# Kernel tuning notes

Hardware: AMD Instinct MI355X
Metric: run time of the kernel (lower is better)

The kernel has to match this reference:

```python
import jax, jax.numpy as jnp
import numpy as np

N_NODES = 100000
N_EDGES = 3200000
N_IN = 512
N_H = 256

def setup_inputs() -> dict:
    key = jax.random.key(0)
    ks = jax.random.split(key, 8)
    features = jax.random.normal(ks[0], (N_NODES, N_IN), dtype=jnp.float32)
    src = jax.random.randint(ks[1], (N_EDGES,), 0, N_NODES, dtype=jnp.int32)
    dst = jax.random.randint(ks[2], (N_EDGES,), 0, N_NODES, dtype=jnp.int32)
    W1 = jax.random.normal(ks[3], (N_IN, N_H), dtype=jnp.float32) / np.sqrt(N_IN)
    b1 = jnp.zeros((N_H,), dtype=jnp.float32)
    a1 = jnp.full((N_H,), 0.25, dtype=jnp.float32)  # PReLU init
    W2 = jax.random.normal(ks[4], (N_H, N_H), dtype=jnp.float32) / np.sqrt(N_H)
    b2 = jnp.zeros((N_H,), dtype=jnp.float32)
    a2 = jnp.full((N_H,), 0.25, dtype=jnp.float32)
    return {"features": features, "src": src, "dst": dst,
            "W1": W1, "b1": b1, "a1": a1, "W2": W2, "b2": b2, "a2": a2}

def _degree_norms(src, dst, n_nodes):
    ones = jnp.ones(src.shape[0], dtype=jnp.float32)
    out_deg = jax.ops.segment_sum(ones, src, num_segments=n_nodes)
    in_deg = jax.ops.segment_sum(ones, dst, num_segments=n_nodes)
    # DGL clamps degree to min 1 for norm='both'
    norm_src = jax.lax.rsqrt(jnp.maximum(out_deg, 1.0))  # [N]
    norm_dst = jax.lax.rsqrt(jnp.maximum(in_deg, 1.0))   # [N]
    return norm_src, norm_dst

def _graph_conv(x, src, dst, norm_src, norm_dst, W, b, a):
    # DGL GraphConv norm='both': h = Dd^-1/2 * A^T (Ds^-1/2 * x W) + b, then PReLU
    h = (x * norm_src[:, None]) @ W                     # [N, out]
    agg = jax.ops.segment_sum(h[src], dst, num_segments=x.shape[0])  # SpMM gather/scatter
    h = agg * norm_dst[:, None] + b
    return jnp.maximum(h, 0.0) + a * jnp.minimum(h, 0.0)  # PReLU per-channel

def reference(features, src, dst, W1, b1, a1, W2, b2, a2):
    norm_src, norm_dst = _degree_norms(src, dst, features.shape[0])
    h = _graph_conv(features, src, dst, norm_src, norm_dst, W1, b1, a1)
    h = _graph_conv(h, src, dst, norm_src, norm_dst, W2, b2, a2)
    return h
```

## Files before the change

kernel.cpp:

```cpp
#include <hip/hip_runtime.h>
#include <hip/hip_bf16.h>

typedef unsigned short u16;
typedef short s16x8 __attribute__((ext_vector_type(8)));
typedef u16 u16x4 __attribute__((ext_vector_type(4)));
typedef u16 u16x8 __attribute__((ext_vector_type(8)));
typedef float f32x4 __attribute__((ext_vector_type(4)));

#define BSHIFT 10

__device__ __forceinline__ u16 f2bf(float f) {
    __hip_bfloat16 b = __float2bfloat16(f);
    return __builtin_bit_cast(u16, b);
}
__device__ __forceinline__ float bf2f(u16 u) {
    unsigned int x = ((unsigned int)u) << 16;
    return __builtin_bit_cast(float, x);
}


__global__ __launch_bounds__(256) void bhist_k(const int* __restrict__ src,
                                               const int* __restrict__ dst,
                                               int* __restrict__ bcntA,
                                               int* __restrict__ bcntB,
                                               int E, int chunk) {
    __shared__ int hA[128], hB[128];
    const int base = blockIdx.x * chunk;
    const int end = (base + chunk) < E ? (base + chunk) : E;
    if (threadIdx.x < 128) { hA[threadIdx.x] = 0; hB[threadIdx.x] = 0; }
    __syncthreads();
    for (int i = base + threadIdx.x; i < end; i += 256) {
        atomicAdd(&hA[dst[i] >> BSHIFT], 1);
        atomicAdd(&hB[src[i] >> BSHIFT], 1);
    }
    __syncthreads();
    if (threadIdx.x < 128) {
        if (hA[threadIdx.x]) atomicAdd(&bcntA[threadIdx.x], hA[threadIdx.x]);
        if (hB[threadIdx.x]) atomicAdd(&bcntB[threadIdx.x], hB[threadIdx.x]);
    }
}

__global__ void bscan_k(const int* __restrict__ bcntA, const int* __restrict__ bcntB,
                        int* __restrict__ bbaseA, int* __restrict__ bbaseB,
                        int* __restrict__ bcurA, int* __restrict__ bcurB,
                        int* __restrict__ row_ptr, int NB, int N, int E) {
    __shared__ int tA[128], tB[128];
    const int t = threadIdx.x;
    int vA = (t < NB) ? bcntA[t] : 0;
    int vB = (t < NB) ? bcntB[t] : 0;
    tA[t] = vA; tB[t] = vB;
    __syncthreads();
    for (int d = 1; d < 128; d <<= 1) {
        int aA = (t >= d) ? tA[t - d] : 0;
        int aB = (t >= d) ? tB[t - d] : 0;
        __syncthreads();
        tA[t] += aA; tB[t] += aB;
        __syncthreads();
    }
    if (t < NB) {
        int eA = tA[t] - vA, eB = tB[t] - vB;
        bbaseA[t] = eA; bcurA[t] = eA;
        bbaseB[t] = eB; bcurB[t] = eB;
    } else if (t == NB) {
        bbaseA[NB] = E; bbaseB[NB] = E;
    }
    if (t == 0) row_ptr[N] = E;
}

__global__ __launch_bounds__(256) void part_k(const int* __restrict__ src,
                                              const int* __restrict__ dst,
                                              int* __restrict__ bcurA,
                                              int* __restrict__ bcurB,
                                              int2* __restrict__ pairs,
                                              int* __restrict__ sb,
                                              int E, int chunk) {
    __shared__ int hA[128], hB[128];
    const int base = blockIdx.x * chunk;
    const int end = (base + chunk) < E ? (base + chunk) : E;
    if (threadIdx.x < 128) { hA[threadIdx.x] = 0; hB[threadIdx.x] = 0; }
    __syncthreads();
    for (int i = base + threadIdx.x; i < end; i += 256) {
        atomicAdd(&hA[dst[i] >> BSHIFT], 1);
        atomicAdd(&hB[src[i] >> BSHIFT], 1);
    }
    __syncthreads();
    if (threadIdx.x < 128) {
        int c = hA[threadIdx.x];
        hA[threadIdx.x] = c ? atomicAdd(&bcurA[threadIdx.x], c) : 0;
        c = hB[threadIdx.x];
        hB[threadIdx.x] = c ? atomicAdd(&bcurB[threadIdx.x], c) : 0;
    }
    __syncthreads();
    for (int i = base + threadIdx.x; i < end; i += 256) {
        int d = dst[i], s = src[i];
        int posA = atomicAdd(&hA[d >> BSHIFT], 1);
        int2 pr; pr.x = s; pr.y = d;
        pairs[posA] = pr;
        int posB = atomicAdd(&hB[s >> BSHIFT], 1);
        sb[posB] = s;
    }
}

__global__ __launch_bounds__(256) void bcsr_k(const int2* __restrict__ pairs,
                                              const int* __restrict__ bbase,
                                              int* __restrict__ row_ptr,
                                              int* __restrict__ din,
                                              int* __restrict__ col, int N) {
    __shared__ int hist[1024];
    __shared__ int cur[1024];
    __shared__ int psum[256];
    const int b = blockIdx.x;
    const int beg = bbase[b], end = bbase[b + 1];
    const int nbase = b << BSHIFT;
    const int nlen = (N - nbase) < 1024 ? (N - nbase) : 1024;
    const int t = threadIdx.x;
#pragma unroll
    for (int j = 0; j < 4; j++) hist[t * 4 + j] = 0;
    __syncthreads();
    for (int i = beg + t; i < end; i += 256)
        atomicAdd(&hist[pairs[i].y - nbase], 1);
    __syncthreads();
    int h0 = hist[4 * t], h1 = hist[4 * t + 1], h2 = hist[4 * t + 2], h3 = hist[4 * t + 3];
    int s = h0 + h1 + h2 + h3;
    psum[t] = s;
    __syncthreads();
    for (int d = 1; d < 256; d <<= 1) {
        int add = (t >= d) ? psum[t - d] : 0;
        __syncthreads();
        psum[t] += add;
        __syncthreads();
    }
    int e0 = psum[t] - s;
    int e1 = e0 + h0, e2 = e1 + h1, e3 = e2 + h2;
    cur[4 * t] = beg + e0; cur[4 * t + 1] = beg + e1;
    cur[4 * t + 2] = beg + e2; cur[4 * t + 3] = beg + e3;
    if (4 * t + 0 < nlen) { row_ptr[nbase + 4 * t + 0] = beg + e0; din[nbase + 4 * t + 0] = h0; }
    if (4 * t + 1 < nlen) { row_ptr[nbase + 4 * t + 1] = beg + e1; din[nbase + 4 * t + 1] = h1; }
    if (4 * t + 2 < nlen) { row_ptr[nbase + 4 * t + 2] = beg + e2; din[nbase + 4 * t + 2] = h2; }
    if (4 * t + 3 < nlen) { row_ptr[nbase + 4 * t + 3] = beg + e3; din[nbase + 4 * t + 3] = h3; }
    __syncthreads();
    for (int i = beg + t; i < end; i += 256) {
        int2 p = pairs[i];
        int pos = atomicAdd(&cur[p.y - nbase], 1);
        col[pos] = p.x;
    }
}

__global__ __launch_bounds__(256) void bdeg_k(const int* __restrict__ sb,
                                              const int* __restrict__ bbase,
                                              int* __restrict__ dout, int N) {
    __shared__ int hist[1024];
    const int b = blockIdx.x;
    const int beg = bbase[b], end = bbase[b + 1];
    const int nbase = b << BSHIFT;
    const int nlen = (N - nbase) < 1024 ? (N - nbase) : 1024;
    for (int i = threadIdx.x; i < 1024; i += 256) hist[i] = 0;
    __syncthreads();
    for (int i = beg + threadIdx.x; i < end; i += 256)
        atomicAdd(&hist[sb[i] - nbase], 1);
    __syncthreads();
    for (int i = threadIdx.x; i < nlen; i += 256) dout[nbase + i] = hist[i];
}

__global__ void norms_k(const int* __restrict__ dout, const int* __restrict__ din,
                        float* __restrict__ ns, float* __restrict__ nd, int n) {
    int i = blockIdx.x * blockDim.x + threadIdx.x;
    if (i < n) {
        ns[i] = 1.0f / sqrtf(fmaxf((float)dout[i], 1.0f));
        nd[i] = 1.0f / sqrtf(fmaxf((float)din[i], 1.0f));
    }
}

__global__ void convt_k(const float* __restrict__ W, u16* __restrict__ Wt, int K, int Nn) {
    int i = blockIdx.x * blockDim.x + threadIdx.x;
    if (i < K * Nn) {
        int n = i / K, k = i - n * K;
        Wt[i] = f2bf(W[(size_t)k * Nn + n]);
    }
}


template <int K, bool AF32>
__global__ __launch_bounds__(256) void gemm_k(const void* __restrict__ Ap,
                                              const float* __restrict__ nsrc,
                                              const u16* __restrict__ Bt,
                                              u16* __restrict__ C, int M) {
    constexpr int BMt = 128, BKt = 64;
    __shared__ u16 Al[BMt * BKt];
    __shared__ u16 Bl[128 * BKt];
    const int tid = threadIdx.x, lane = tid & 63, wid = tid >> 6;
    const int wr = wid >> 1, wc = wid & 1;
    const int l15 = lane & 15, lhi = lane >> 4;
    const int bm = blockIdx.x * BMt, bn = blockIdx.y * 128;
    f32x4 acc[4][4] = {};

    for (int k0 = 0; k0 < K; k0 += BKt) {
#pragma unroll
        for (int i = 0; i < 4; i++) {
            int G = i * 256 + tid, row = G >> 3, gk = G & 7;
            int grow = bm + row;
            grow = grow < M ? grow : M - 1;
            u16x8 w;
            if constexpr (AF32) {
                const float* A = (const float*)Ap;
                const f32x4 v0 = *(const f32x4*)(A + (size_t)grow * K + k0 + gk * 8);
                const f32x4 v1 = *(const f32x4*)(A + (size_t)grow * K + k0 + gk * 8 + 4);
                const float ns = nsrc[grow];
                w[0] = f2bf(v0[0] * ns); w[1] = f2bf(v0[1] * ns);
                w[2] = f2bf(v0[2] * ns); w[3] = f2bf(v0[3] * ns);
                w[4] = f2bf(v1[0] * ns); w[5] = f2bf(v1[1] * ns);
                w[6] = f2bf(v1[2] * ns); w[7] = f2bf(v1[3] * ns);
            } else {
                const u16* A = (const u16*)Ap;
                w = *(const u16x8*)(A + (size_t)grow * K + k0 + gk * 8);
            }
            int idx = (row * BKt + gk * 8) ^ ((row & 7) << 3);
            *(u16x8*)(Al + idx) = w;
            u16x8 wb = *(const u16x8*)(Bt + (size_t)(bn + row) * K + k0 + gk * 8);
            *(u16x8*)(Bl + idx) = wb;
        }
        __syncthreads();

        s16x8 af[2][4], bfr[2][4];
#pragma unroll
        for (int kk = 0; kk < 2; kk++) {
#pragma unroll
            for (int mi = 0; mi < 4; mi++) {
                int row = wr * 64 + mi * 16 + l15;
                int idx = (row * BKt + kk * 32 + lhi * 8) ^ ((row & 7) << 3);
                af[kk][mi] = *(const s16x8*)(Al + idx);
            }
#pragma unroll
            for (int ni = 0; ni < 4; ni++) {
                int n = wc * 64 + ni * 16 + l15;
                int idx = (n * BKt + kk * 32 + lhi * 8) ^ ((n & 7) << 3);
                bfr[kk][ni] = *(const s16x8*)(Bl + idx);
            }
        }
#pragma unroll
        for (int kk = 0; kk < 2; kk++)
#pragma unroll
            for (int mi = 0; mi < 4; mi++)
#pragma unroll
                for (int ni = 0; ni < 4; ni++)
                    acc[mi][ni] = __builtin_amdgcn_mfma_f32_16x16x32_bf16(
                        af[kk][mi], bfr[kk][ni], acc[mi][ni], 0, 0, 0);
        __syncthreads();
    }

#pragma unroll
    for (int mi = 0; mi < 4; mi++) {
#pragma unroll
        for (int r = 0; r < 4; r++) {
            int grow = bm + wr * 64 + mi * 16 + lhi * 4 + r;
            if (grow < M) {
#pragma unroll
                for (int ni = 0; ni < 4; ni++) {
                    int gcol = bn + wc * 64 + ni * 16 + l15;
                    C[(size_t)grow * 256 + gcol] = f2bf(acc[mi][ni][r]);
                }
            }
        }
    }
}


__global__ __launch_bounds__(256) void agg_k(const u16* __restrict__ h,
                                             const int* __restrict__ rp,
                                             const int* __restrict__ col,
                                             const float* __restrict__ nd,
                                             const float* __restrict__ bias,
                                             const float* __restrict__ alpha,
                                             const float* __restrict__ ns,
                                             u16* __restrict__ obf, float* __restrict__ of,
                                             int n) {
    int w = (blockIdx.x * blockDim.x + threadIdx.x) >> 6;
    if (w >= n) return;
    const int lane = threadIdx.x & 63;
    const int half = lane >> 5, c0 = (lane & 31) * 8;
    const int beg = rp[w], end = rp[w + 1];

    float a0[8] = {}, a1[8] = {}, a2[8] = {}, a3[8] = {};

    int p = beg + half;
    for (; p + 6 < end; p += 8) {
        int s0 = col[p], s1 = col[p + 2], s2 = col[p + 4], s3 = col[p + 6];
        u16x8 v0 = *(const u16x8*)(h + (size_t)s0 * 256 + c0);
        u16x8 v1 = *(const u16x8*)(h + (size_t)s1 * 256 + c0);
        u16x8 v2 = *(const u16x8*)(h + (size_t)s2 * 256 + c0);
        u16x8 v3 = *(const u16x8*)(h + (size_t)s3 * 256 + c0);
#pragma unroll
        for (int j = 0; j < 8; j++) {
            a0[j] += bf2f(v0[j]);
            a1[j] += bf2f(v1[j]);
            a2[j] += bf2f(v2[j]);
            a3[j] += bf2f(v3[j]);
        }
    }
    for (; p < end; p += 2) {
        int s = col[p];
        u16x8 v = *(const u16x8*)(h + (size_t)s * 256 + c0);
#pragma unroll
        for (int j = 0; j < 8; j++) a0[j] += bf2f(v[j]);
    }
#pragma unroll
    for (int j = 0; j < 8; j++) a0[j] += (a1[j] + a2[j]) + a3[j];
#pragma unroll
    for (int j = 0; j < 8; j++) a0[j] += __shfl_xor(a0[j], 32);

    const float ndv = nd[w];
    const f32x4 bv0 = *(const f32x4*)(bias + c0);
    const f32x4 bv1 = *(const f32x4*)(bias + c0 + 4);
    const f32x4 al0 = *(const f32x4*)(alpha + c0);
    const f32x4 al1 = *(const f32x4*)(alpha + c0 + 4);
    float bb[8] = {bv0[0], bv0[1], bv0[2], bv0[3], bv1[0], bv1[1], bv1[2], bv1[3]};
    float aa[8] = {al0[0], al0[1], al0[2], al0[3], al1[0], al1[1], al1[2], al1[3]};
#pragma unroll
    for (int j = 0; j < 8; j++) {
        float s = a0[j] * ndv + bb[j];
        a0[j] = s > 0.f ? s : aa[j] * s;
    }

    if (half == 0) {
        if (obf) {
            const float nsv = ns[w];
            u16x8 o;
#pragma unroll
            for (int j = 0; j < 8; j++) o[j] = f2bf(a0[j] * nsv);
            *(u16x8*)(obf + (size_t)w * 256 + c0) = o;
        } else {
            f32x4 o0, o1;
            o0[0] = a0[0]; o0[1] = a0[1]; o0[2] = a0[2]; o0[3] = a0[3];
            o1[0] = a0[4]; o1[1] = a0[5]; o1[2] = a0[6]; o1[3] = a0[7];
            *(f32x4*)(of + (size_t)w * 256 + c0) = o0;
            *(f32x4*)(of + (size_t)w * 256 + c0 + 4) = o1;
        }
    }
}


extern "C" void kernel_launch(void* const* d_in, const int* in_sizes, int n_in,
                              void* d_out, int out_size, void* d_ws, size_t ws_size,
                              hipStream_t stream) {
    const float* feat = (const float*)d_in[0];
    const int* src = (const int*)d_in[1];
    const int* dst = (const int*)d_in[2];
    const float* W1 = (const float*)d_in[3];
    const float* b1 = (const float*)d_in[4];
    const float* a1 = (const float*)d_in[5];
    const float* W2 = (const float*)d_in[6];
    const float* b2 = (const float*)d_in[7];
    const float* a2 = (const float*)d_in[8];
    float* out = (float*)d_out;

    const int N = in_sizes[0] / 512;
    const int E = in_sizes[1];
    const int NB = (N + (1 << BSHIFT) - 1) >> BSHIFT;

    char* ws = (char*)d_ws;
    size_t off = 0;
    auto take = [&](size_t bytes) {
        size_t o = off;
        off += (bytes + 255) & ~(size_t)255;
        return o;
    };
    int* deg_out = (int*)(ws + take((size_t)N * 4));
    int* deg_in = (int*)(ws + take((size_t)N * 4));
    float* nsrc = (float*)(ws + take((size_t)N * 4));
    float* ndst = (float*)(ws + take((size_t)N * 4));
    int* row_ptr = (int*)(ws + take((size_t)(N + 1) * 4));
    int* bcnt = (int*)(ws + take(1024));
    int* bcntA = bcnt, * bcntB = bcnt + 128;
    int* bbaseA = (int*)(ws + take(512));
    int* bbaseB = (int*)(ws + take(512));
    int* bcurA = (int*)(ws + take(512));
    int* bcurB = (int*)(ws + take(512));
    int* col = (int*)(ws + take((size_t)E * 4));
    u16* W1t = (u16*)(ws + take((size_t)512 * 256 * 2));
    u16* W2t = (u16*)(ws + take((size_t)256 * 256 * 2));
    u16* h = (u16*)(ws + take((size_t)N * 256 * 2));
    u16* x2 = (u16*)(ws + take((size_t)N * 256 * 2));
    int2* pairs = (int2*)h;
    int* sb = (int*)x2;

    hipMemsetAsync(bcnt, 0, 1024, stream);

    const int chunk = 4096;
    bhist_k<<<(E + chunk - 1) / chunk, 256, 0, stream>>>(src, dst, bcntA, bcntB, E, chunk);
    bscan_k<<<1, 128, 0, stream>>>(bcntA, bcntB, bbaseA, bbaseB, bcurA, bcurB, row_ptr, NB, N, E);
    part_k<<<(E + chunk - 1) / chunk, 256, 0, stream>>>(src, dst, bcurA, bcurB, pairs, sb, E, chunk);
    bcsr_k<<<NB, 256, 0, stream>>>(pairs, bbaseA, row_ptr, deg_in, col, N);
    bdeg_k<<<NB, 256, 0, stream>>>(sb, bbaseB, deg_out, N);
    norms_k<<<(N + 255) / 256, 256, 0, stream>>>(deg_out, deg_in, nsrc, ndst, N);

    convt_k<<<(512 * 256 + 255) / 256, 256, 0, stream>>>(W1, W1t, 512, 256);
    convt_k<<<(256 * 256 + 255) / 256, 256, 0, stream>>>(W2, W2t, 256, 256);

    dim3 gg((N + 127) / 128, 2);
    int aggBlocks = (N * 64 + 255) / 256;

    gemm_k<512, true><<<gg, 256, 0, stream>>>(feat, nsrc, W1t, h, N);
    agg_k<<<aggBlocks, 256, 0, stream>>>(h, row_ptr, col, ndst, b1, a1, nsrc, x2, nullptr, N);
    gemm_k<256, false><<<gg, 256, 0, stream>>>(x2, nullptr, W2t, h, N);
    agg_k<<<aggBlocks, 256, 0, stream>>>(h, row_ptr, col, ndst, b2, a2, nullptr, nullptr, out, N);
}
```

Measured before the change: 759.3 us.

## Widen GEMM tile to full N and use half-wave per node in aggregation

```diff
diff --git a/kernel.cpp b/kernel.cpp
--- a/kernel.cpp
+++ b/kernel.cpp
@@ -181,23 +181,23 @@
 
 
 template <int K, bool AF32>
-__global__ __launch_bounds__(256) void gemm_k(const void* __restrict__ Ap,
+__global__ __launch_bounds__(512) void gemm_k(const void* __restrict__ Ap,
                                               const float* __restrict__ nsrc,
                                               const u16* __restrict__ Bt,
                                               u16* __restrict__ C, int M) {
-    constexpr int BMt = 128, BKt = 64;
-    __shared__ u16 Al[BMt * BKt];
-    __shared__ u16 Bl[128 * BKt];
+    constexpr int BKt = 64;
+    __shared__ u16 Al[128 * BKt];
+    __shared__ u16 Bl[256 * BKt];
     const int tid = threadIdx.x, lane = tid & 63, wid = tid >> 6;
-    const int wr = wid >> 1, wc = wid & 1;
+    const int wr = wid >> 2, wc = wid & 3;
     const int l15 = lane & 15, lhi = lane >> 4;
-    const int bm = blockIdx.x * BMt, bn = blockIdx.y * 128;
+    const int bm = blockIdx.x * 128;
     f32x4 acc[4][4] = {};
 
     for (int k0 = 0; k0 < K; k0 += BKt) {
 #pragma unroll
-        for (int i = 0; i < 4; i++) {
-            int G = i * 256 + tid, row = G >> 3, gk = G & 7;
+        for (int i = 0; i < 2; i++) {
+            int G = i * 512 + tid, row = G >> 3, gk = G & 7;
             int grow = bm + row;
             grow = grow < M ? grow : M - 1;
             u16x8 w;
@@ -216,7 +216,12 @@
             }
             int idx = (row * BKt + gk * 8) ^ ((row & 7) << 3);
             *(u16x8*)(Al + idx) = w;
-            u16x8 wb = *(const u16x8*)(Bt + (size_t)(bn + row) * K + k0 + gk * 8);
+        }
+#pragma unroll
+        for (int i = 0; i < 4; i++) {
+            int G = i * 512 + tid, row = G >> 3, gk = G & 7;
+            u16x8 wb = *(const u16x8*)(Bt + (size_t)row * K + k0 + gk * 8);
+            int idx = (row * BKt + gk * 8) ^ ((row & 7) << 3);
             *(u16x8*)(Bl + idx) = wb;
         }
         __syncthreads();
@@ -256,7 +261,7 @@
             if (grow < M) {
 #pragma unroll
                 for (int ni = 0; ni < 4; ni++) {
-                    int gcol = bn + wc * 64 + ni * 16 + l15;
+                    int gcol = wc * 64 + ni * 16 + l15;
                     C[(size_t)grow * 256 + gcol] = f2bf(acc[mi][ni][r]);
                 }
             }
@@ -274,21 +279,25 @@
                                              const float* __restrict__ ns,
                                              u16* __restrict__ obf, float* __restrict__ of,
                                              int n) {
-    int w = (blockIdx.x * blockDim.x + threadIdx.x) >> 6;
+    int w = (blockIdx.x * blockDim.x + threadIdx.x) >> 5;
     if (w >= n) return;
-    const int lane = threadIdx.x & 63;
-    const int half = lane >> 5, c0 = (lane & 31) * 8;
+    const int c0 = (threadIdx.x & 31) * 8;
     const int beg = rp[w], end = rp[w + 1];
 
     float a0[8] = {}, a1[8] = {}, a2[8] = {}, a3[8] = {};
 
-    int p = beg + half;
-    for (; p + 6 < end; p += 8) {
-        int s0 = col[p], s1 = col[p + 2], s2 = col[p + 4], s3 = col[p + 6];
+    int p = beg;
+    for (; p + 7 < end; p += 8) {
+        int s0 = col[p], s1 = col[p + 1], s2 = col[p + 2], s3 = col[p + 3];
+        int s4 = col[p + 4], s5 = col[p + 5], s6 = col[p + 6], s7 = col[p + 7];
         u16x8 v0 = *(const u16x8*)(h + (size_t)s0 * 256 + c0);
         u16x8 v1 = *(const u16x8*)(h + (size_t)s1 * 256 + c0);
         u16x8 v2 = *(const u16x8*)(h + (size_t)s2 * 256 + c0);
         u16x8 v3 = *(const u16x8*)(h + (size_t)s3 * 256 + c0);
+        u16x8 v4 = *(const u16x8*)(h + (size_t)s4 * 256 + c0);
+        u16x8 v5 = *(const u16x8*)(h + (size_t)s5 * 256 + c0);
+        u16x8 v6 = *(const u16x8*)(h + (size_t)s6 * 256 + c0);
+        u16x8 v7 = *(const u16x8*)(h + (size_t)s7 * 256 + c0);
 #pragma unroll
         for (int j = 0; j < 8; j++) {
             a0[j] += bf2f(v0[j]);
@@ -296,17 +305,36 @@
             a2[j] += bf2f(v2[j]);
             a3[j] += bf2f(v3[j]);
         }
-    }
-    for (; p < end; p += 2) {
+#pragma unroll
+        for (int j = 0; j < 8; j++) {
+            a0[j] += bf2f(v4[j]);
+            a1[j] += bf2f(v5[j]);
+            a2[j] += bf2f(v6[j]);
+            a3[j] += bf2f(v7[j]);
+        }
+    }
+    for (; p + 3 < end; p += 4) {
+        int s0 = col[p], s1 = col[p + 1], s2 = col[p + 2], s3 = col[p + 3];
+        u16x8 v0 = *(const u16x8*)(h + (size_t)s0 * 256 + c0);
+        u16x8 v1 = *(const u16x8*)(h + (size_t)s1 * 256 + c0);
+        u16x8 v2 = *(const u16x8*)(h + (size_t)s2 * 256 + c0);
+        u16x8 v3 = *(const u16x8*)(h + (size_t)s3 * 256 + c0);
+#pragma unroll
+        for (int j = 0; j < 8; j++) {
+            a0[j] += bf2f(v0[j]);
+            a1[j] += bf2f(v1[j]);
+            a2[j] += bf2f(v2[j]);
+            a3[j] += bf2f(v3[j]);
+        }
+    }
+    for (; p < end; p++) {
         int s = col[p];
         u16x8 v = *(const u16x8*)(h + (size_t)s * 256 + c0);
 #pragma unroll
         for (int j = 0; j < 8; j++) a0[j] += bf2f(v[j]);
     }
 #pragma unroll
-    for (int j = 0; j < 8; j++) a0[j] += (a1[j] + a2[j]) + a3[j];
-#pragma unroll
-    for (int j = 0; j < 8; j++) a0[j] += __shfl_xor(a0[j], 32);
+    for (int j = 0; j < 8; j++) a0[j] = (a0[j] + a1[j]) + (a2[j] + a3[j]);
 
     const float ndv = nd[w];
     const f32x4 bv0 = *(const f32x4*)(bias + c0);
@@ -321,20 +349,18 @@
         a0[j] = s > 0.f ? s : aa[j] * s;
     }
 
-    if (half == 0) {
-        if (obf) {
-            const float nsv = ns[w];
-            u16x8 o;
-#pragma unroll
-            for (int j = 0; j < 8; j++) o[j] = f2bf(a0[j] * nsv);
-            *(u16x8*)(obf + (size_t)w * 256 + c0) = o;
-        } else {
-            f32x4 o0, o1;
-            o0[0] = a0[0]; o0[1] = a0[1]; o0[2] = a0[2]; o0[3] = a0[3];
-            o1[0] = a0[4]; o1[1] = a0[5]; o1[2] = a0[6]; o1[3] = a0[7];
-            *(f32x4*)(of + (size_t)w * 256 + c0) = o0;
-            *(f32x4*)(of + (size_t)w * 256 + c0 + 4) = o1;
-        }
+    if (obf) {
+        const float nsv = ns[w];
+        u16x8 o;
+#pragma unroll
+        for (int j = 0; j < 8; j++) o[j] = f2bf(a0[j] * nsv);
+        *(u16x8*)(obf + (size_t)w * 256 + c0) = o;
+    } else {
+        f32x4 o0, o1;
+        o0[0] = a0[0]; o0[1] = a0[1]; o0[2] = a0[2]; o0[3] = a0[3];
+        o1[0] = a0[4]; o1[1] = a0[5]; o1[2] = a0[6]; o1[3] = a0[7];
+        *(f32x4*)(of + (size_t)w * 256 + c0) = o0;
+        *(f32x4*)(of + (size_t)w * 256 + c0 + 4) = o1;
     }
 }
 
@@ -396,11 +422,11 @@
     convt_k<<<(512 * 256 + 255) / 256, 256, 0, stream>>>(W1, W1t, 512, 256);
     convt_k<<<(256 * 256 + 255) / 256, 256, 0, stream>>>(W2, W2t, 256, 256);
 
-    dim3 gg((N + 127) / 128, 2);
-    int aggBlocks = (N * 64 + 255) / 256;
-
-    gemm_k<512, true><<<gg, 256, 0, stream>>>(feat, nsrc, W1t, h, N);
+    dim3 gg((N + 127) / 128);
+    int aggBlocks = (N * 32 + 255) / 256;
+
+    gemm_k<512, true><<<gg, 512, 0, stream>>>(feat, nsrc, W1t, h, N);
     agg_k<<<aggBlocks, 256, 0, stream>>>(h, row_ptr, col, ndst, b1, a1, nsrc, x2, nullptr, N);
-    gemm_k<256, false><<<gg, 256, 0, stream>>>(x2, nullptr, W2t, h, N);
+    gemm_k<256, false><<<gg, 512, 0, stream>>>(x2, nullptr, W2t, h, N);
     agg_k<<<aggBlocks, 256, 0, stream>>>(h, row_ptr, col, ndst, b2, a2, nullptr, nullptr, out, N);
 }
```

Measured after the change: 761.5 us. No clear change (+0.3%).
